# Performance work log

Hardware: AMD Instinct MI355X
Metric: run time of the kernel (lower is better)

## Reference

```python
import itertools
import jax, jax.numpy as jnp
import numpy as np

N_SLOTS = 8  # = n_parts (square assignment, so Hungarian == optimal permutation)
PERMS = jnp.asarray(list(itertools.permutations(range(N_SLOTS))), dtype=jnp.int32)  # (8!, 8)
ROWS = jnp.arange(N_SLOTS)[None, :]  # (1, 8)
LOG_CLAMP = -100.0  # torch F.binary_cross_entropy clamps log terms at -100
EPS = 1e-4


def setup_inputs() -> dict:
    key = jax.random.key(0)
    k1, k2, k3, k4 = jax.random.split(key, 4)
    B, S, N, A = 16, N_SLOTS, 131072, 18
    # pred seg mask holds log-probabilities (torch.exp is applied before BCE)
    pred_seg_logp = jnp.log(jax.random.uniform(k1, (B, S, N), minval=EPS, maxval=1.0 - EPS))
    # pred affordance holds probabilities (fed to BCE directly)
    pred_aff = jax.random.uniform(k2, (B, S, A), minval=EPS, maxval=1.0 - EPS)
    gt_seg_mask = jax.random.randint(k3, (B, N), 0, S, dtype=jnp.int32)
    gt_aff = jax.random.randint(k4, (B, S, A), 0, 2, dtype=jnp.int32)
    return {"pred_seg_logp": pred_seg_logp, "pred_aff": pred_aff,
            "gt_seg_mask": gt_seg_mask, "gt_aff": gt_aff}


def _bce_cost_matrix(log_p, log_1mp, g):
    # cost[b,i,j] = mean_k BCE(p[b,i,k], g[b,j,k]); g is binary {0,1}
    # = -( sum_k g[b,j,k]*log_p[b,i,k] + sum_k (1-g[b,j,k])*log_1mp[b,i,k] ) / K
    K = log_p.shape[-1]
    t1 = jnp.einsum('bik,bjk->bij', log_p, g)
    t2 = jnp.einsum('bik,bjk->bij', log_1mp, 1.0 - g)
    return -(t1 + t2) / K


def _min_assignment_loss(cost):
    # cost: (B, S, S). Optimal assignment via brute force over permutations
    # (equivalent to linear_sum_assignment for square matrices), then
    # sum of matched costs averaged over batch.
    pc = cost[:, ROWS, PERMS].sum(-1)  # (B, 8!)
    return jnp.min(pc, axis=1).mean()


def reference(pred_seg_logp, pred_aff, gt_seg_mask, gt_aff):
    B, S, N = pred_seg_logp.shape
    # one-hot gt parts: (B, n_parts, N)
    g_seg = (gt_seg_mask[:, None, :] == jnp.arange(S)[None, :, None]).astype(jnp.float32)
    # BCE(exp(logp), g): log(p) = logp, log(1-p) = log1p(-exp(logp)), both clamped
    lgp = jnp.maximum(pred_seg_logp, LOG_CLAMP)
    lg1m = jnp.maximum(jnp.log1p(-jnp.exp(pred_seg_logp)), LOG_CLAMP)
    seg_cost = _bce_cost_matrix(lgp, lg1m, g_seg)  # (B, S, S)
    seg_loss = _min_assignment_loss(seg_cost)

    g_aff = gt_aff.astype(jnp.float32)
    lgp_a = jnp.maximum(jnp.log(pred_aff), LOG_CLAMP)
    lg1m_a = jnp.maximum(jnp.log1p(-pred_aff), LOG_CLAMP)
    aff_cost = _bce_cost_matrix(lgp_a, lg1m_a, g_aff)  # (B, S, S)
    aff_loss = _min_assignment_loss(aff_cost)

    loss = aff_loss + 3.0 * seg_loss
    return jnp.stack([seg_loss, aff_loss, loss])
```

## Files before the change

kernel.cpp:

```cpp
#include <hip/hip_runtime.h>

#define NB 16
#define NS 8
#define NPTS 131072
#define NA 18
#define CHUNKS 16
#define ELEMS (NPTS / CHUNKS)
#define THREADS 256
#define GROUPS (ELEMS / 4 / THREADS)

#define WS_SP 0
#define WS_T  (NB * NS * NS)
#define WS_SUMS (WS_T + NB * NS)
#define WS_FLOATS (WS_SUMS + 2)

__device__ __forceinline__ void proc_elem(float x, int m, float acc[8], float& tsum) {
    float lgp  = fmaxf(x, -100.0f);
    float e    = __expf(x);
    float lg1m = fmaxf(__logf(1.0f - e), -100.0f);
    float d    = lgp - lg1m;
    tsum += lg1m;
#pragma unroll
    for (int j = 0; j < 8; ++j) acc[j] += (m == j) ? d : 0.0f;
}

__global__ __launch_bounds__(THREADS) void seg_accum_kernel(
    const float* __restrict__ logp, const int* __restrict__ mask,
    float* __restrict__ ws) {
    const int chunk = blockIdx.x;
    const int i = blockIdx.y;
    const int b = blockIdx.z;
    const size_t roff = ((size_t)(b * NS + i)) * NPTS + (size_t)chunk * ELEMS;
    const float4* lp4 = (const float4*)(logp + roff);
    const int4*   m4  = (const int4*)(mask + (size_t)b * NPTS + (size_t)chunk * ELEMS);

    float acc[8] = {0.f, 0.f, 0.f, 0.f, 0.f, 0.f, 0.f, 0.f};
    float tsum = 0.f;

#pragma unroll
    for (int g = 0; g < GROUPS; ++g) {
        const int idx = g * THREADS + (int)threadIdx.x;
        const float4 lp = lp4[idx];
        const int4   mm = m4[idx];
        proc_elem(lp.x, mm.x, acc, tsum);
        proc_elem(lp.y, mm.y, acc, tsum);
        proc_elem(lp.z, mm.z, acc, tsum);
        proc_elem(lp.w, mm.w, acc, tsum);
    }

#pragma unroll
    for (int off = 32; off > 0; off >>= 1) {
#pragma unroll
        for (int j = 0; j < 8; ++j) acc[j] += __shfl_down(acc[j], off);
        tsum += __shfl_down(tsum, off);
    }

    __shared__ float red[THREADS / 64][9];
    const int wave = threadIdx.x >> 6;
    const int lane = threadIdx.x & 63;
    if (lane == 0) {
#pragma unroll
        for (int j = 0; j < 8; ++j) red[wave][j] = acc[j];
        red[wave][8] = tsum;
    }
    __syncthreads();
    if (threadIdx.x < 9) {
        float v = red[0][threadIdx.x] + red[1][threadIdx.x] +
                  red[2][threadIdx.x] + red[3][threadIdx.x];
        if (threadIdx.x < 8)
            atomicAdd(&ws[WS_SP + ((b * NS + i) * NS) + threadIdx.x], v);
        else
            atomicAdd(&ws[WS_T + b * NS + i], v);
    }
}

__global__ __launch_bounds__(64) void assign_kernel(
    const float* __restrict__ ws_in, const float* __restrict__ pred_aff,
    const int* __restrict__ gt_aff, float* __restrict__ sums) {
    const int bw = blockIdx.x;
    const int b = bw >> 1;
    const int w = bw & 1;
    const int lane = threadIdx.x;
    const int i = lane >> 3, j = lane & 7;

    __shared__ float cost[8][8];
    __shared__ float dp[256];

    float c;
    if (w == 0) {
        c = -(ws_in[WS_SP + ((b * NS + i) * NS) + j] + ws_in[WS_T + b * NS + i]) *
            (1.0f / (float)NPTS);
    } else {
        float a = 0.f;
#pragma unroll
        for (int k = 0; k < NA; ++k) {
            float p = pred_aff[((b * NS + i) * NA) + k];
            float g = (float)gt_aff[((b * NS + j) * NA) + k];
            float lgp  = fmaxf(__logf(p), -100.0f);
            float l1m  = fmaxf(__logf(1.0f - p), -100.0f);
            a += g * lgp + (1.0f - g) * l1m;
        }
        c = -a * (1.0f / (float)NA);
    }
    cost[i][j] = c;

    dp[lane] = 1e30f; dp[lane + 64] = 1e30f; dp[lane + 128] = 1e30f; dp[lane + 192] = 1e30f;
    __syncthreads();
    if (lane == 0) dp[0] = 0.f;
    __syncthreads();

    for (int l = 1; l <= 8; ++l) {
#pragma unroll
        for (int base = 0; base < 256; base += 64) {
            const int mm = base + lane;
            if (__popc(mm) == l) {
                float best = 1e30f;
#pragma unroll
                for (int jj = 0; jj < 8; ++jj) {
                    if (mm & (1 << jj))
                        best = fminf(best, dp[mm ^ (1 << jj)] + cost[l - 1][jj]);
                }
                dp[mm] = best;
            }
        }
        __syncthreads();
    }
    if (lane == 0) atomicAdd(&sums[w], dp[255] * (1.0f / (float)NB));
}

__global__ void writeout_kernel(const float* __restrict__ sums, float* __restrict__ out) {
    const float seg = sums[0], aff = sums[1];
    out[0] = seg;
    out[1] = aff;
    out[2] = aff + 3.0f * seg;
}

extern "C" void kernel_launch(void* const* d_in, const int* in_sizes, int n_in,
                              void* d_out, int out_size, void* d_ws, size_t ws_size,
                              hipStream_t stream) {
    const float* pred_seg_logp = (const float*)d_in[0];
    const float* pred_aff      = (const float*)d_in[1];
    const int*   gt_seg_mask   = (const int*)d_in[2];
    const int*   gt_aff        = (const int*)d_in[3];
    float* out = (float*)d_out;
    float* ws  = (float*)d_ws;

    hipMemsetAsync(ws, 0, WS_FLOATS * sizeof(float), stream);

    dim3 grid(CHUNKS, NS, NB);
    seg_accum_kernel<<<grid, THREADS, 0, stream>>>(pred_seg_logp, gt_seg_mask, ws);
    assign_kernel<<<NB * 2, 64, 0, stream>>>(ws, pred_aff, gt_aff, ws + WS_SUMS);
    writeout_kernel<<<1, 1, 0, stream>>>(ws + WS_SUMS, out);
}
```

Before: 124.4 us.

## Process all slots per block to reuse mask loads and drop atomics and memset

Each block now covers one batch and one chunk for all 8 slots. Lane groups of 8 handle different slots over the same points, so the mask is read once per block rather than once per slot. Partials go to per-chunk workspace slots instead of atomics, which removes the memset. The assign and writeout kernels now do a deterministic reduction over chunks and batches. In exchange, each warp's loads are split into 8 separate 128-byte row segments, and the assign kernel runs a serial loop over 64 chunk partials.

```diff
diff --git a/kernel.cpp b/kernel.cpp
--- a/kernel.cpp
+++ b/kernel.cpp
@@ -4,15 +4,16 @@
 #define NS 8
 #define NPTS 131072
 #define NA 18
-#define CHUNKS 16
+
+#define THREADS 256
+#define WAVES (THREADS / 64)
+#define CHUNKS 64
 #define ELEMS (NPTS / CHUNKS)
-#define THREADS 256
-#define GROUPS (ELEMS / 4 / THREADS)
+#define PT_PER_WAVE (ELEMS / WAVES)
+#define ITERS (PT_PER_WAVE / 32)
 
-#define WS_SP 0
-#define WS_T  (NB * NS * NS)
-#define WS_SUMS (WS_T + NB * NS)
-#define WS_FLOATS (WS_SUMS + 2)
+#define PARTIALS 72
+#define WS_RES (NB * CHUNKS * PARTIALS)
 
 __device__ __forceinline__ void proc_elem(float x, int m, float acc[8], float& tsum) {
     float lgp  = fmaxf(x, -100.0f);
@@ -28,59 +29,60 @@
     const float* __restrict__ logp, const int* __restrict__ mask,
     float* __restrict__ ws) {
     const int chunk = blockIdx.x;
-    const int i = blockIdx.y;
-    const int b = blockIdx.z;
-    const size_t roff = ((size_t)(b * NS + i)) * NPTS + (size_t)chunk * ELEMS;
-    const float4* lp4 = (const float4*)(logp + roff);
-    const int4*   m4  = (const int4*)(mask + (size_t)b * NPTS + (size_t)chunk * ELEMS);
+    const int b = blockIdx.y;
+    const int tid = (int)threadIdx.x;
+    const int wave = tid >> 6;
+    const int lane = tid & 63;
+    const int g = lane >> 3;
+    const int t = lane & 7;
+
+    const int ptbase = chunk * ELEMS + wave * PT_PER_WAVE;
+    const int4*   m4  = (const int4*)(mask + (size_t)b * NPTS + ptbase);
+    const float4* lp4 = (const float4*)(logp + ((size_t)(b * NS + g)) * NPTS + ptbase);
 
     float acc[8] = {0.f, 0.f, 0.f, 0.f, 0.f, 0.f, 0.f, 0.f};
-    float tsum = 0.f;
+    float ts = 0.f;
 
 #pragma unroll
-    for (int g = 0; g < GROUPS; ++g) {
-        const int idx = g * THREADS + (int)threadIdx.x;
+    for (int it = 0; it < ITERS; ++it) {
+        const int idx = it * 8 + t;
+        const int4   mm = m4[idx];
         const float4 lp = lp4[idx];
-        const int4   mm = m4[idx];
-        proc_elem(lp.x, mm.x, acc, tsum);
-        proc_elem(lp.y, mm.y, acc, tsum);
-        proc_elem(lp.z, mm.z, acc, tsum);
-        proc_elem(lp.w, mm.w, acc, tsum);
+        proc_elem(lp.x, mm.x, acc, ts);
+        proc_elem(lp.y, mm.y, acc, ts);
+        proc_elem(lp.z, mm.z, acc, ts);
+        proc_elem(lp.w, mm.w, acc, ts);
     }
 
 #pragma unroll
-    for (int off = 32; off > 0; off >>= 1) {
+    for (int off = 4; off > 0; off >>= 1) {
 #pragma unroll
         for (int j = 0; j < 8; ++j) acc[j] += __shfl_down(acc[j], off);
-        tsum += __shfl_down(tsum, off);
+        ts += __shfl_down(ts, off);
     }
 
-    __shared__ float red[THREADS / 64][9];
-    const int wave = threadIdx.x >> 6;
-    const int lane = threadIdx.x & 63;
-    if (lane == 0) {
+    __shared__ float red[WAVES][NS][9];
+    if (t == 0) {
 #pragma unroll
-        for (int j = 0; j < 8; ++j) red[wave][j] = acc[j];
-        red[wave][8] = tsum;
+        for (int j = 0; j < 8; ++j) red[wave][g][j] = acc[j];
+        red[wave][g][8] = ts;
     }
     __syncthreads();
-    if (threadIdx.x < 9) {
-        float v = red[0][threadIdx.x] + red[1][threadIdx.x] +
-                  red[2][threadIdx.x] + red[3][threadIdx.x];
-        if (threadIdx.x < 8)
-            atomicAdd(&ws[WS_SP + ((b * NS + i) * NS) + threadIdx.x], v);
-        else
-            atomicAdd(&ws[WS_T + b * NS + i], v);
+
+    if (tid < PARTIALS) {
+        const int gg = tid / 9, jj = tid % 9;
+        float v = red[0][gg][jj] + red[1][gg][jj] + red[2][gg][jj] + red[3][gg][jj];
+        ws[((size_t)(b * CHUNKS + chunk)) * PARTIALS + tid] = v;
     }
 }
 
 __global__ __launch_bounds__(64) void assign_kernel(
-    const float* __restrict__ ws_in, const float* __restrict__ pred_aff,
-    const int* __restrict__ gt_aff, float* __restrict__ sums) {
+    const float* __restrict__ parts, const float* __restrict__ pred_aff,
+    const int* __restrict__ gt_aff, float* __restrict__ res) {
     const int bw = blockIdx.x;
     const int b = bw >> 1;
     const int w = bw & 1;
-    const int lane = threadIdx.x;
+    const int lane = (int)threadIdx.x;
     const int i = lane >> 3, j = lane & 7;
 
     __shared__ float cost[8][8];
@@ -88,16 +90,21 @@
 
     float c;
     if (w == 0) {
-        c = -(ws_in[WS_SP + ((b * NS + i) * NS) + j] + ws_in[WS_T + b * NS + i]) *
-            (1.0f / (float)NPTS);
+        float sp = 0.f, tt = 0.f;
+        for (int cch = 0; cch < CHUNKS; ++cch) {
+            const float* p = parts + ((size_t)(b * CHUNKS + cch)) * PARTIALS;
+            sp += p[i * 9 + j];
+            tt += p[i * 9 + 8];
+        }
+        c = -(sp + tt) * (1.0f / (float)NPTS);
     } else {
         float a = 0.f;
 #pragma unroll
         for (int k = 0; k < NA; ++k) {
             float p = pred_aff[((b * NS + i) * NA) + k];
             float g = (float)gt_aff[((b * NS + j) * NA) + k];
-            float lgp  = fmaxf(__logf(p), -100.0f);
-            float l1m  = fmaxf(__logf(1.0f - p), -100.0f);
+            float lgp = fmaxf(__logf(p), -100.0f);
+            float l1m = fmaxf(__logf(1.0f - p), -100.0f);
             a += g * lgp + (1.0f - g) * l1m;
         }
         c = -a * (1.0f / (float)NA);
@@ -125,14 +132,27 @@
         }
         __syncthreads();
     }
-    if (lane == 0) atomicAdd(&sums[w], dp[255] * (1.0f / (float)NB));
+    if (lane == 0) res[bw] = dp[255];
 }
 
-__global__ void writeout_kernel(const float* __restrict__ sums, float* __restrict__ out) {
-    const float seg = sums[0], aff = sums[1];
-    out[0] = seg;
-    out[1] = aff;
-    out[2] = aff + 3.0f * seg;
+__global__ __launch_bounds__(64) void writeout_kernel(
+    const float* __restrict__ res, float* __restrict__ out) {
+    const int lane = (int)threadIdx.x;
+    float v = (lane < 2 * NB) ? res[lane] : 0.f;
+    float segv = ((lane & 1) == 0) ? v : 0.f;
+    float affv = ((lane & 1) == 1) ? v : 0.f;
+#pragma unroll
+    for (int off = 32; off > 0; off >>= 1) {
+        segv += __shfl_down(segv, off);
+        affv += __shfl_down(affv, off);
+    }
+    if (lane == 0) {
+        const float seg = segv * (1.0f / (float)NB);
+        const float aff = affv * (1.0f / (float)NB);
+        out[0] = seg;
+        out[1] = aff;
+        out[2] = aff + 3.0f * seg;
+    }
 }
 
 extern "C" void kernel_launch(void* const* d_in, const int* in_sizes, int n_in,
@@ -145,10 +165,8 @@
     float* out = (float*)d_out;
     float* ws  = (float*)d_ws;
 
-    hipMemsetAsync(ws, 0, WS_FLOATS * sizeof(float), stream);
-
-    dim3 grid(CHUNKS, NS, NB);
+    dim3 grid(CHUNKS, NB);
     seg_accum_kernel<<<grid, THREADS, 0, stream>>>(pred_seg_logp, gt_seg_mask, ws);
-    assign_kernel<<<NB * 2, 64, 0, stream>>>(ws, pred_aff, gt_aff, ws + WS_SUMS);
-    writeout_kernel<<<1, 1, 0, stream>>>(ws + WS_SUMS, out);
+    assign_kernel<<<NB * 2, 64, 0, stream>>>(ws, pred_aff, gt_aff, ws + WS_RES);
+    writeout_kernel<<<1, 64, 0, stream>>>(ws + WS_RES, out);
 }
```

Measured after the change: 124.8 us. No clear change (+0.3%).
